# Performance work log

Measured on AMD Instinct MI355X. Metric: run time of the kernel, lower is better.

Reference implementation:

```python
import jax, jax.numpy as jnp
import numpy as np

B, C, L = 8, 64, 65536  # batch, channels, flattened H*W
GN_EPS = 1e-5


def setup_inputs() -> dict:
    key = jax.random.key(0)
    ks = jax.random.split(key, 8)
    return {
        "x": jax.random.normal(ks[0], (B, C, L), dtype=jnp.float32),
        "inj0": jax.random.normal(ks[1], (B, C, L), dtype=jnp.float32),
        "inj1": jax.random.normal(ks[2], (B, C, L), dtype=jnp.float32),
        "residual": jax.random.normal(ks[3], (B, C, L), dtype=jnp.float32),
        "gate_w": jax.random.normal(ks[4], (C, C), dtype=jnp.float32) * (1.0 / np.sqrt(C)),
        "gate_b": jax.random.normal(ks[5], (C,), dtype=jnp.float32) * 0.01,
        "fuse_w": jax.random.normal(ks[6], (C, C), dtype=jnp.float32) * (1.0 / np.sqrt(C)),
        "fuse_b": jax.random.normal(ks[7], (C,), dtype=jnp.float32) * 0.01,
        "gn_w": jnp.ones((C,), dtype=jnp.float32),
        "gn_b": jnp.zeros((C,), dtype=jnp.float32),
    }


def _conv1x1(w, b, t):
    # Conv1d with kernel_size=1: [O,C] x [B,C,L] -> [B,O,L]
    return jnp.einsum('oc,bcl->bol', w, t) + b[None, :, None]


def reference(x, inj0, inj1, residual, gate_w, gate_b, fuse_w, fuse_b, gn_w, gn_b):
    # per-injection gate + elementwise multiply, summed over injections
    acc = jnp.zeros_like(x)
    for inj in (inj0, inj1):  # fixed small list of injection features
        acc = acc + x * _conv1x1(gate_w, gate_b, inj + x)
    # fuse conv + residual + ReLU (dropout p=0 -> identity)
    out = jax.nn.relu(_conv1x1(fuse_w, fuse_b, acc) + residual)
    # GroupNorm(num_groups=1): normalize over (C, L) per sample, per-channel affine
    mean = jnp.mean(out, axis=(1, 2), keepdims=True)
    var = jnp.var(out, axis=(1, 2), keepdims=True)
    out = (out - mean) * jax.lax.rsqrt(var + GN_EPS)
    return out * gn_w[None, :, None] + gn_b[None, :, None]
```

## Files before the change

kernel.cpp:

```cpp
#include <hip/hip_runtime.h>
#include <stdint.h>

#define Bv 8
#define Cv 64
#define Lv 65536
#define TPB 512
#define COLS 256
#define BLKS_PER_B (Lv / COLS)
#define GRID1 (Bv * BLKS_PER_B)


typedef __attribute__((ext_vector_type(8))) short short8;
typedef __attribute__((ext_vector_type(4))) float f32x4;

#define SSTRIDE 260

__device__ __forceinline__ uint16_t f2bf(float f) {
    uint32_t u = __float_as_uint(f);
    uint32_t r = u + 0x7FFFu + ((u >> 16) & 1u);
    return (uint16_t)(r >> 16);
}
__device__ __forceinline__ uint32_t pack2bf(float lo, float hi) {
    return (uint32_t)f2bf(lo) | ((uint32_t)f2bf(hi) << 16);
}

__global__ void pass1(const float* __restrict__ x, const float* __restrict__ inj0,
                      const float* __restrict__ inj1, const float* __restrict__ resid,
                      const float* __restrict__ gate_w, const float* __restrict__ gate_b,
                      const float* __restrict__ fuse_w, const float* __restrict__ fuse_b,
                      float* __restrict__ out, float* __restrict__ partials)
{
    __shared__ uint32_t s_buf[32 * SSTRIDE];
    __shared__ uint32_t a_buf[16 * SSTRIDE];
    __shared__ uint32_t w_lds[2][64][36];
    __shared__ float cinit[2][64];
    __shared__ float wred[16];

    const int tid  = threadIdx.x;
    const int lane = tid & 63;
    const int w    = tid >> 6;
    const int g    = lane >> 4;
    const int ln   = lane & 15;

    const int b    = blockIdx.x >> 8;
    const int lb   = blockIdx.x & 255;
    const int col0 = lb * COLS;
    const int bCL  = b * (Cv * Lv);

    {
        const int mat = tid >> 8;
        const int m   = (tid >> 2) & 63;
        const int k0  = (tid & 3) << 4;
        const float* wsrc = mat ? fuse_w : gate_w;
        const float4* w4 = reinterpret_cast<const float4*>(wsrc + m * 64 + k0);
        uint32_t* dst = &w_lds[mat][m][k0 >> 1];
        #pragma unroll
        for (int q = 0; q < 4; ++q) {
            const float4 v = w4[q];
            dst[2 * q]     = pack2bf(v.x, v.y);
            dst[2 * q + 1] = pack2bf(v.z, v.w);
        }
        if (tid < 64) {
            cinit[0][tid] = 2.0f * gate_b[tid];
            cinit[1][tid] = fuse_b[tid];
        }
    }

    #pragma unroll
    for (int uu = 0; uu < 4; ++uu) {
        const int u  = tid + uu * TPB;
        const int kp = u >> 6;
        const int c  = (u & 63) << 2;
        const int rA = bCL + (2 * kp) * Lv + col0 + c;
        const int rB = rA + Lv;
        const float4 xA = *reinterpret_cast<const float4*>(x    + rA);
        const float4 aA = *reinterpret_cast<const float4*>(inj0 + rA);
        const float4 bA = *reinterpret_cast<const float4*>(inj1 + rA);
        const float4 xB = *reinterpret_cast<const float4*>(x    + rB);
        const float4 aB = *reinterpret_cast<const float4*>(inj0 + rB);
        const float4 bB = *reinterpret_cast<const float4*>(inj1 + rB);
        uint4 dw;
        dw.x = pack2bf(aA.x + bA.x + 2.0f * xA.x, aB.x + bB.x + 2.0f * xB.x);
        dw.y = pack2bf(aA.y + bA.y + 2.0f * xA.y, aB.y + bB.y + 2.0f * xB.y);
        dw.z = pack2bf(aA.z + bA.z + 2.0f * xA.z, aB.z + bB.z + 2.0f * xB.z);
        dw.w = pack2bf(aA.w + bA.w + 2.0f * xA.w, aB.w + bB.w + 2.0f * xB.w);
        *reinterpret_cast<uint4*>(&s_buf[kp * SSTRIDE + c]) = dw;
    }
    __syncthreads();

    f32x4 D2[4][2];
    #pragma unroll
    for (int oc = 0; oc < 4; ++oc) {
        const float4 cb = *reinterpret_cast<const float4*>(&cinit[1][16 * oc + 4 * g]);
        D2[oc][0][0] = cb.x; D2[oc][0][1] = cb.y;
        D2[oc][0][2] = cb.z; D2[oc][0][3] = cb.w;
        D2[oc][1] = D2[oc][0];
    }

    float lsum = 0.0f, lsq = 0.0f;

    #pragma unroll 1
    for (int ph = 0; ph < 2; ++ph) {
        f32x4 D1[2][2];
        #pragma unroll
        for (int o2 = 0; o2 < 2; ++o2) {
            const int oc = 2 * ph + o2;
            const float4 cb = *reinterpret_cast<const float4*>(&cinit[0][16 * oc + 4 * g]);
            D1[o2][0][0] = cb.x; D1[o2][0][1] = cb.y;
            D1[o2][0][2] = cb.z; D1[o2][0][3] = cb.w;
            D1[o2][1] = D1[o2][0];
        }
        #pragma unroll
        for (int nt = 0; nt < 2; ++nt) {
            const int n = ln + 16 * (2 * w + nt);
            uint4 B0, B1;
            B0.x = s_buf[(4 * g + 0) * SSTRIDE + n];
            B0.y = s_buf[(4 * g + 1) * SSTRIDE + n];
            B0.z = s_buf[(4 * g + 2) * SSTRIDE + n];
            B0.w = s_buf[(4 * g + 3) * SSTRIDE + n];
            B1.x = s_buf[(16 + 4 * g + 0) * SSTRIDE + n];
            B1.y = s_buf[(16 + 4 * g + 1) * SSTRIDE + n];
            B1.z = s_buf[(16 + 4 * g + 2) * SSTRIDE + n];
            B1.w = s_buf[(16 + 4 * g + 3) * SSTRIDE + n];
            #pragma unroll
            for (int o2 = 0; o2 < 2; ++o2) {
                const int m = ln + 16 * (2 * ph + o2);
                const uint4 A0 = *reinterpret_cast<const uint4*>(&w_lds[0][m][4 * g]);
                const uint4 A1 = *reinterpret_cast<const uint4*>(&w_lds[0][m][16 + 4 * g]);
                D1[o2][nt] = __builtin_amdgcn_mfma_f32_16x16x32_bf16(
                    __builtin_bit_cast(short8, A0), __builtin_bit_cast(short8, B0),
                    D1[o2][nt], 0, 0, 0);
                D1[o2][nt] = __builtin_amdgcn_mfma_f32_16x16x32_bf16(
                    __builtin_bit_cast(short8, A1), __builtin_bit_cast(short8, B1),
                    D1[o2][nt], 0, 0, 0);
            }
        }

        #pragma unroll
        for (int nt = 0; nt < 2; ++nt) {
            const int n  = ln + 16 * (2 * w + nt);
            const int cg = bCL + col0 + n;
            #pragma unroll
            for (int o2 = 0; o2 < 2; ++o2) {
                const int m0 = 16 * (2 * ph + o2) + 4 * g;
                float av[4];
                #pragma unroll
                for (int j = 0; j < 4; ++j)
                    av[j] = x[cg + (m0 + j) * Lv] * D1[o2][nt][j];
                const int kpA = 8 * o2 + 2 * g;
                a_buf[kpA * SSTRIDE + n]       = pack2bf(av[0], av[1]);
                a_buf[(kpA + 1) * SSTRIDE + n] = pack2bf(av[2], av[3]);
            }
        }
        __syncthreads();

        #pragma unroll
        for (int nt = 0; nt < 2; ++nt) {
            const int n = ln + 16 * (2 * w + nt);
            uint4 Bf;
            Bf.x = a_buf[(4 * g + 0) * SSTRIDE + n];
            Bf.y = a_buf[(4 * g + 1) * SSTRIDE + n];
            Bf.z = a_buf[(4 * g + 2) * SSTRIDE + n];
            Bf.w = a_buf[(4 * g + 3) * SSTRIDE + n];
            #pragma unroll
            for (int oc = 0; oc < 4; ++oc) {
                const int m = ln + 16 * oc;
                const uint4 A = *reinterpret_cast<const uint4*>(&w_lds[1][m][16 * ph + 4 * g]);
                D2[oc][nt] = __builtin_amdgcn_mfma_f32_16x16x32_bf16(
                    __builtin_bit_cast(short8, A), __builtin_bit_cast(short8, Bf),
                    D2[oc][nt], 0, 0, 0);
            }
        }
        __syncthreads();
    }

    {
        float* uf = reinterpret_cast<float*>(a_buf);
        const int rowin = tid >> 5;
        const int cl    = tid & 31;
        #pragma unroll
        for (int ck = 0; ck < 4; ++ck) {
            #pragma unroll
            for (int nt = 0; nt < 2; ++nt) {
                const int n = ln + 16 * (2 * w + nt);
                #pragma unroll
                for (int j = 0; j < 4; ++j)
                    uf[(4 * g + j) * SSTRIDE + n] = D2[ck][nt][j];
            }
            const int m   = 16 * ck + rowin;
            const int gbm = bCL + m * Lv + col0;
            const float4 ra = *reinterpret_cast<const float4*>(&resid[gbm + 4 * cl]);
            const float4 rb = *reinterpret_cast<const float4*>(&resid[gbm + 4 * cl + 128]);
            __syncthreads();
            float4 va = *reinterpret_cast<const float4*>(&uf[rowin * SSTRIDE + 4 * cl]);
            float4 vb = *reinterpret_cast<const float4*>(&uf[rowin * SSTRIDE + 4 * cl + 128]);
            va.x = fmaxf(va.x + ra.x, 0.0f); va.y = fmaxf(va.y + ra.y, 0.0f);
            va.z = fmaxf(va.z + ra.z, 0.0f); va.w = fmaxf(va.w + ra.w, 0.0f);
            vb.x = fmaxf(vb.x + rb.x, 0.0f); vb.y = fmaxf(vb.y + rb.y, 0.0f);
            vb.z = fmaxf(vb.z + rb.z, 0.0f); vb.w = fmaxf(vb.w + rb.w, 0.0f);
            *reinterpret_cast<float4*>(&out[gbm + 4 * cl])       = va;
            *reinterpret_cast<float4*>(&out[gbm + 4 * cl + 128]) = vb;
            lsum += (va.x + va.y) + (va.z + va.w) + (vb.x + vb.y) + (vb.z + vb.w);
            lsq = fmaf(va.x, va.x, lsq); lsq = fmaf(va.y, va.y, lsq);
            lsq = fmaf(va.z, va.z, lsq); lsq = fmaf(va.w, va.w, lsq);
            lsq = fmaf(vb.x, vb.x, lsq); lsq = fmaf(vb.y, vb.y, lsq);
            lsq = fmaf(vb.z, vb.z, lsq); lsq = fmaf(vb.w, vb.w, lsq);
            __syncthreads();
        }
    }

    #pragma unroll
    for (int st = 1; st < 64; st <<= 1) {
        lsum += __shfl_xor(lsum, st);
        lsq  += __shfl_xor(lsq,  st);
    }
    if (lane == 0) { wred[2 * w] = lsum; wred[2 * w + 1] = lsq; }
    __syncthreads();
    if (tid == 0) {
        float s = 0.0f, q = 0.0f;
        #pragma unroll
        for (int i = 0; i < 8; ++i) { s += wred[2 * i]; q += wred[2 * i + 1]; }
        partials[2 * blockIdx.x]     = s;
        partials[2 * blockIdx.x + 1] = q;
    }
}

__global__ __launch_bounds__(256)
void pass2(const float* __restrict__ partials, const float* __restrict__ gn_w,
           const float* __restrict__ gn_b, float* __restrict__ sb)
{
    __shared__ float r1[256], r2[256];
    __shared__ float mean_s, rs_s;
    const int b = blockIdx.x, tid = threadIdx.x;
    r1[tid] = partials[2 * (b * 256 + tid)];
    r2[tid] = partials[2 * (b * 256 + tid) + 1];
    __syncthreads();
    #pragma unroll
    for (int st = 128; st > 0; st >>= 1) {
        if (tid < st) { r1[tid] += r1[tid + st]; r2[tid] += r2[tid + st]; }
        __syncthreads();
    }
    if (tid == 0) {
        const float n = (float)Cv * (float)Lv;
        const float mean = r1[0] / n;
        const float var  = r2[0] / n - mean * mean;
        mean_s = mean;
        rs_s   = rsqrtf(var + 1e-5f);
    }
    __syncthreads();
    if (tid < Cv) {
        const float sc = gn_w[tid] * rs_s;
        sb[b * Cv + tid]           = sc;
        sb[Bv * Cv + b * Cv + tid] = fmaf(-mean_s, sc, gn_b[tid]);
    }
// ... 48 lines not shown
```

Measured before the change: 187.5 us.

## Process each block's columns in two halves to shrink LDS and registers

The 256-column tile per block is now processed as two sequential 128-column halves. Each wave owns one 16-column slice, and the separate a_buf is dropped by reusing s_buf for the intermediate product and the output staging. LDS use roughly halves and accumulator registers shrink, which should allow more resident blocks per CU to hide memory latency on this bandwidth-bound kernel. The cost is more barriers per block and less independent MFMA work per wave within each half.

```diff
diff --git a/kernel.cpp b/kernel.cpp
--- a/kernel.cpp
+++ b/kernel.cpp
@@ -5,6 +5,7 @@
 #define Cv 64
 #define Lv 65536
 #define TPB 512
+#define HALF 128
 #define COLS 256
 #define BLKS_PER_B (Lv / COLS)
 #define GRID1 (Bv * BLKS_PER_B)
@@ -13,7 +14,7 @@
 typedef __attribute__((ext_vector_type(8))) short short8;
 typedef __attribute__((ext_vector_type(4))) float f32x4;
 
-#define SSTRIDE 260
+#define SSTRIDE 132
 
 __device__ __forceinline__ uint16_t f2bf(float f) {
     uint32_t u = __float_as_uint(f);
@@ -31,7 +32,6 @@
                       float* __restrict__ out, float* __restrict__ partials)
 {
     __shared__ uint32_t s_buf[32 * SSTRIDE];
-    __shared__ uint32_t a_buf[16 * SSTRIDE];
     __shared__ uint32_t w_lds[2][64][36];
     __shared__ float cinit[2][64];
     __shared__ float wred[16];
@@ -41,10 +41,10 @@
     const int w    = tid >> 6;
     const int g    = lane >> 4;
     const int ln   = lane & 15;
+    const int n    = 16 * w + ln;
 
     const int b    = blockIdx.x >> 8;
     const int lb   = blockIdx.x & 255;
-    const int col0 = lb * COLS;
     const int bCL  = b * (Cv * Lv);
 
     {
@@ -66,53 +66,41 @@
         }
     }
 
-    #pragma unroll
-    for (int uu = 0; uu < 4; ++uu) {
-        const int u  = tid + uu * TPB;
-        const int kp = u >> 6;
-        const int c  = (u & 63) << 2;
-        const int rA = bCL + (2 * kp) * Lv + col0 + c;
-        const int rB = rA + Lv;
-        const float4 xA = *reinterpret_cast<const float4*>(x    + rA);
-        const float4 aA = *reinterpret_cast<const float4*>(inj0 + rA);
-        const float4 bA = *reinterpret_cast<const float4*>(inj1 + rA);
-        const float4 xB = *reinterpret_cast<const float4*>(x    + rB);
-        const float4 aB = *reinterpret_cast<const float4*>(inj0 + rB);
-        const float4 bB = *reinterpret_cast<const float4*>(inj1 + rB);
-        uint4 dw;
-        dw.x = pack2bf(aA.x + bA.x + 2.0f * xA.x, aB.x + bB.x + 2.0f * xB.x);
-        dw.y = pack2bf(aA.y + bA.y + 2.0f * xA.y, aB.y + bB.y + 2.0f * xB.y);
-        dw.z = pack2bf(aA.z + bA.z + 2.0f * xA.z, aB.z + bB.z + 2.0f * xB.z);
-        dw.w = pack2bf(aA.w + bA.w + 2.0f * xA.w, aB.w + bB.w + 2.0f * xB.w);
-        *reinterpret_cast<uint4*>(&s_buf[kp * SSTRIDE + c]) = dw;
-    }
-    __syncthreads();
-
-    f32x4 D2[4][2];
-    #pragma unroll
-    for (int oc = 0; oc < 4; ++oc) {
-        const float4 cb = *reinterpret_cast<const float4*>(&cinit[1][16 * oc + 4 * g]);
-        D2[oc][0][0] = cb.x; D2[oc][0][1] = cb.y;
-        D2[oc][0][2] = cb.z; D2[oc][0][3] = cb.w;
-        D2[oc][1] = D2[oc][0];
-    }
-
     float lsum = 0.0f, lsq = 0.0f;
 
     #pragma unroll 1
-    for (int ph = 0; ph < 2; ++ph) {
-        f32x4 D1[2][2];
-        #pragma unroll
-        for (int o2 = 0; o2 < 2; ++o2) {
-            const int oc = 2 * ph + o2;
+    for (int h = 0; h < 2; ++h) {
+        const int col0 = lb * COLS + h * HALF;
+
+        #pragma unroll
+        for (int uu = 0; uu < 2; ++uu) {
+            const int u  = tid + uu * TPB;
+            const int kp = u >> 5;
+            const int c  = (u & 31) << 2;
+            const int rA = bCL + (2 * kp) * Lv + col0 + c;
+            const int rB = rA + Lv;
+            const float4 xA = *reinterpret_cast<const float4*>(x    + rA);
+            const float4 aA = *reinterpret_cast<const float4*>(inj0 + rA);
+            const float4 bA = *reinterpret_cast<const float4*>(inj1 + rA);
+            const float4 xB = *reinterpret_cast<const float4*>(x    + rB);
+            const float4 aB = *reinterpret_cast<const float4*>(inj0 + rB);
+            const float4 bB = *reinterpret_cast<const float4*>(inj1 + rB);
+            uint4 dw;
+            dw.x = pack2bf(aA.x + bA.x + 2.0f * xA.x, aB.x + bB.x + 2.0f * xB.x);
+            dw.y = pack2bf(aA.y + bA.y + 2.0f * xA.y, aB.y + bB.y + 2.0f * xB.y);
+            dw.z = pack2bf(aA.z + bA.z + 2.0f * xA.z, aB.z + bB.z + 2.0f * xB.z);
+            dw.w = pack2bf(aA.w + bA.w + 2.0f * xA.w, aB.w + bB.w + 2.0f * xB.w);
+            *reinterpret_cast<uint4*>(&s_buf[kp * SSTRIDE + c]) = dw;
+        }
+        __syncthreads();
+
+        f32x4 D1[4];
+        #pragma unroll
+        for (int oc = 0; oc < 4; ++oc) {
             const float4 cb = *reinterpret_cast<const float4*>(&cinit[0][16 * oc + 4 * g]);
-            D1[o2][0][0] = cb.x; D1[o2][0][1] = cb.y;
-            D1[o2][0][2] = cb.z; D1[o2][0][3] = cb.w;
-            D1[o2][1] = D1[o2][0];
-        }
-        #pragma unroll
-        for (int nt = 0; nt < 2; ++nt) {
-            const int n = ln + 16 * (2 * w + nt);
+            D1[oc][0] = cb.x; D1[oc][1] = cb.y; D1[oc][2] = cb.z; D1[oc][3] = cb.w;
+        }
+        {
             uint4 B0, B1;
             B0.x = s_buf[(4 * g + 0) * SSTRIDE + n];
             B0.y = s_buf[(4 * g + 1) * SSTRIDE + n];
@@ -123,89 +111,99 @@
             B1.z = s_buf[(16 + 4 * g + 2) * SSTRIDE + n];
             B1.w = s_buf[(16 + 4 * g + 3) * SSTRIDE + n];
             #pragma unroll
-            for (int o2 = 0; o2 < 2; ++o2) {
-                const int m = ln + 16 * (2 * ph + o2);
+            for (int oc = 0; oc < 4; ++oc) {
+                const int m = ln + 16 * oc;
                 const uint4 A0 = *reinterpret_cast<const uint4*>(&w_lds[0][m][4 * g]);
                 const uint4 A1 = *reinterpret_cast<const uint4*>(&w_lds[0][m][16 + 4 * g]);
-                D1[o2][nt] = __builtin_amdgcn_mfma_f32_16x16x32_bf16(
+                D1[oc] = __builtin_amdgcn_mfma_f32_16x16x32_bf16(
                     __builtin_bit_cast(short8, A0), __builtin_bit_cast(short8, B0),
-                    D1[o2][nt], 0, 0, 0);
-                D1[o2][nt] = __builtin_amdgcn_mfma_f32_16x16x32_bf16(
+                    D1[oc], 0, 0, 0);
+                D1[oc] = __builtin_amdgcn_mfma_f32_16x16x32_bf16(
                     __builtin_bit_cast(short8, A1), __builtin_bit_cast(short8, B1),
-                    D1[o2][nt], 0, 0, 0);
+                    D1[oc], 0, 0, 0);
             }
         }
 
-        #pragma unroll
-        for (int nt = 0; nt < 2; ++nt) {
-            const int n  = ln + 16 * (2 * w + nt);
+        {
             const int cg = bCL + col0 + n;
             #pragma unroll
-            for (int o2 = 0; o2 < 2; ++o2) {
-                const int m0 = 16 * (2 * ph + o2) + 4 * g;
+            for (int oc = 0; oc < 4; ++oc) {
+                const int m0 = 16 * oc + 4 * g;
                 float av[4];
                 #pragma unroll
                 for (int j = 0; j < 4; ++j)
-                    av[j] = x[cg + (m0 + j) * Lv] * D1[o2][nt][j];
-                const int kpA = 8 * o2 + 2 * g;
-                a_buf[kpA * SSTRIDE + n]       = pack2bf(av[0], av[1]);
-                a_buf[(kpA + 1) * SSTRIDE + n] = pack2bf(av[2], av[3]);
+                    av[j] = x[cg + (m0 + j) * Lv] * D1[oc][j];
+                const int kp = 8 * oc + 2 * g;
+                s_buf[kp * SSTRIDE + n]       = pack2bf(av[0], av[1]);
+                s_buf[(kp + 1) * SSTRIDE + n] = pack2bf(av[2], av[3]);
             }
         }
         __syncthreads();
 
-        #pragma unroll
-        for (int nt = 0; nt < 2; ++nt) {
-            const int n = ln + 16 * (2 * w + nt);
-            uint4 Bf;
-            Bf.x = a_buf[(4 * g + 0) * SSTRIDE + n];
-            Bf.y = a_buf[(4 * g + 1) * SSTRIDE + n];
-            Bf.z = a_buf[(4 * g + 2) * SSTRIDE + n];
-            Bf.w = a_buf[(4 * g + 3) * SSTRIDE + n];
+        f32x4 D2[4];
+        #pragma unroll
+        for (int oc = 0; oc < 4; ++oc) {
+            const float4 cb = *reinterpret_cast<const float4*>(&cinit[1][16 * oc + 4 * g]);
+            D2[oc][0] = cb.x; D2[oc][1] = cb.y; D2[oc][2] = cb.z; D2[oc][3] = cb.w;
+        }
+        {
+            uint4 B0, B1;
+            B0.x = s_buf[(4 * g + 0) * SSTRIDE + n];
+            B0.y = s_buf[(4 * g + 1) * SSTRIDE + n];
+            B0.z = s_buf[(4 * g + 2) * SSTRIDE + n];
+            B0.w = s_buf[(4 * g + 3) * SSTRIDE + n];
+            B1.x = s_buf[(16 + 4 * g + 0) * SSTRIDE + n];
+            B1.y = s_buf[(16 + 4 * g + 1) * SSTRIDE + n];
+            B1.z = s_buf[(16 + 4 * g + 2) * SSTRIDE + n];
+            B1.w = s_buf[(16 + 4 * g + 3) * SSTRIDE + n];
             #pragma unroll
             for (int oc = 0; oc < 4; ++oc) {
                 const int m = ln + 16 * oc;
-                const uint4 A = *reinterpret_cast<const uint4*>(&w_lds[1][m][16 * ph + 4 * g]);
-                D2[oc][nt] = __builtin_amdgcn_mfma_f32_16x16x32_bf16(
-                    __builtin_bit_cast(short8, A), __builtin_bit_cast(short8, Bf),
-                    D2[oc][nt], 0, 0, 0);
+                const uint4 A0 = *reinterpret_cast<const uint4*>(&w_lds[1][m][4 * g]);
+                const uint4 A1 = *reinterpret_cast<const uint4*>(&w_lds[1][m][16 + 4 * g]);
+                D2[oc] = __builtin_amdgcn_mfma_f32_16x16x32_bf16(
+                    __builtin_bit_cast(short8, A0), __builtin_bit_cast(short8, B0),
+                    D2[oc], 0, 0, 0);
+                D2[oc] = __builtin_amdgcn_mfma_f32_16x16x32_bf16(
+                    __builtin_bit_cast(short8, A1), __builtin_bit_cast(short8, B1),
+                    D2[oc], 0, 0, 0);
             }
         }
         __syncthreads();
-    }
-
-    {
-        float* uf = reinterpret_cast<float*>(a_buf);
-        const int rowin = tid >> 5;
-        const int cl    = tid & 31;
-        #pragma unroll
-        for (int ck = 0; ck < 4; ++ck) {
-            #pragma unroll
-            for (int nt = 0; nt < 2; ++nt) {
-                const int n = ln + 16 * (2 * w + nt);
+
+        {
+            float* uf = reinterpret_cast<float*>(s_buf);
+            const int rowin = tid >> 4;
+            const int cl    = tid & 15;
+            #pragma unroll 1
+            for (int ck = 0; ck < 2; ++ck) {
                 #pragma unroll
-                for (int j = 0; j < 4; ++j)
-                    uf[(4 * g + j) * SSTRIDE + n] = D2[ck][nt][j];
+                for (int oc2 = 0; oc2 < 2; ++oc2) {
+                    const int oc = 2 * ck + oc2;
+                    #pragma unroll
+                    for (int j = 0; j < 4; ++j)
+                        uf[(16 * oc2 + 4 * g + j) * SSTRIDE + n] = D2[oc][j];
+                }
+                const int m   = 32 * ck + rowin;
+                const int gbm = bCL + m * Lv + col0;
+                const float4 ra = *reinterpret_cast<const float4*>(&resid[gbm + 4 * cl]);
+                const float4 rb = *reinterpret_cast<const float4*>(&resid[gbm + 4 * cl + 64]);
+                __syncthreads();
+                float4 va = *reinterpret_cast<const float4*>(&uf[rowin * SSTRIDE + 4 * cl]);
+                float4 vb = *reinterpret_cast<const float4*>(&uf[rowin * SSTRIDE + 4 * cl + 64]);
+                va.x = fmaxf(va.x + ra.x, 0.0f); va.y = fmaxf(va.y + ra.y, 0.0f);
+                va.z = fmaxf(va.z + ra.z, 0.0f); va.w = fmaxf(va.w + ra.w, 0.0f);
+                vb.x = fmaxf(vb.x + rb.x, 0.0f); vb.y = fmaxf(vb.y + rb.y, 0.0f);
+                vb.z = fmaxf(vb.z + rb.z, 0.0f); vb.w = fmaxf(vb.w + rb.w, 0.0f);
+                *reinterpret_cast<float4*>(&out[gbm + 4 * cl])      = va;
+                *reinterpret_cast<float4*>(&out[gbm + 4 * cl + 64]) = vb;
+                lsum += (va.x + va.y) + (va.z + va.w) + (vb.x + vb.y) + (vb.z + vb.w);
+                lsq = fmaf(va.x, va.x, lsq); lsq = fmaf(va.y, va.y, lsq);
+                lsq = fmaf(va.z, va.z, lsq); lsq = fmaf(va.w, va.w, lsq);
+                lsq = fmaf(vb.x, vb.x, lsq); lsq = fmaf(vb.y, vb.y, lsq);
+                lsq = fmaf(vb.z, vb.z, lsq); lsq = fmaf(vb.w, vb.w, lsq);
+                __syncthreads();
             }
-            const int m   = 16 * ck + rowin;
-            const int gbm = bCL + m * Lv + col0;
-            const float4 ra = *reinterpret_cast<const float4*>(&resid[gbm + 4 * cl]);
-            const float4 rb = *reinterpret_cast<const float4*>(&resid[gbm + 4 * cl + 128]);
-            __syncthreads();
-            float4 va = *reinterpret_cast<const float4*>(&uf[rowin * SSTRIDE + 4 * cl]);
-            float4 vb = *reinterpret_cast<const float4*>(&uf[rowin * SSTRIDE + 4 * cl + 128]);
-            va.x = fmaxf(va.x + ra.x, 0.0f); va.y = fmaxf(va.y + ra.y, 0.0f);
-            va.z = fmaxf(va.z + ra.z, 0.0f); va.w = fmaxf(va.w + ra.w, 0.0f);
-            vb.x = fmaxf(vb.x + rb.x, 0.0f); vb.y = fmaxf(vb.y + rb.y, 0.0f);
-            vb.z = fmaxf(vb.z + rb.z, 0.0f); vb.w = fmaxf(vb.w + rb.w, 0.0f);
-            *reinterpret_cast<float4*>(&out[gbm + 4 * cl])       = va;
-            *reinterpret_cast<float4*>(&out[gbm + 4 * cl + 128]) = vb;
-            lsum += (va.x + va.y) + (va.z + va.w) + (vb.x + vb.y) + (vb.z + vb.w);
-            lsq = fmaf(va.x, va.x, lsq); lsq = fmaf(va.y, va.y, lsq);
-            lsq = fmaf(va.z, va.z, lsq); lsq = fmaf(va.w, va.w, lsq);
-            lsq = fmaf(vb.x, vb.x, lsq); lsq = fmaf(vb.y, vb.y, lsq);
-            lsq = fmaf(vb.z, vb.z, lsq); lsq = fmaf(vb.w, vb.w, lsq);
-            __syncthreads();
         }
     }
 
```

Measured after the change: 191.4 us. 1.02x slower.

## Halve block size, process two column halves per block, load weights from global

Applied to the files above, without the earlier changes.

Cuts the block from 512 to 256 threads. Each block now handles its 256 columns in two 128-column halves, so the LDS tiles shrink to a 132-word stride. The bf16 weight tile in LDS is removed; each wave instead loads its MFMA A fragments directly from global gate_w/fuse_w (cached) and converts them to bf16 per phase. The goal is lower LDS use and higher occupancy, at the cost of repeated global weight loads and conversions and a serialized loop over the two halves.

```diff
diff --git a/kernel.cpp b/kernel.cpp
--- a/kernel.cpp
+++ b/kernel.cpp
@@ -4,7 +4,8 @@
 #define Bv 8
 #define Cv 64
 #define Lv 65536
-#define TPB 512
+#define TPB 256
+#define HALF 128
 #define COLS 256
 #define BLKS_PER_B (Lv / COLS)
 #define GRID1 (Bv * BLKS_PER_B)
@@ -13,7 +14,7 @@
 typedef __attribute__((ext_vector_type(8))) short short8;
 typedef __attribute__((ext_vector_type(4))) float f32x4;
 
-#define SSTRIDE 260
+#define SSTRIDE 132
 
 __device__ __forceinline__ uint16_t f2bf(float f) {
     uint32_t u = __float_as_uint(f);
@@ -22,6 +23,16 @@
 }
 __device__ __forceinline__ uint32_t pack2bf(float lo, float hi) {
     return (uint32_t)f2bf(lo) | ((uint32_t)f2bf(hi) << 16);
+}
+__device__ __forceinline__ uint4 load_wfrag(const float* wp) {
+    const float4 f0 = *reinterpret_cast<const float4*>(wp);
+    const float4 f1 = *reinterpret_cast<const float4*>(wp + 4);
+    uint4 r;
+    r.x = pack2bf(f0.x, f0.y);
+    r.y = pack2bf(f0.z, f0.w);
+    r.z = pack2bf(f1.x, f1.y);
+    r.w = pack2bf(f1.z, f1.w);
+    return r;
 }
 
 __global__ void pass1(const float* __restrict__ x, const float* __restrict__ inj0,
@@ -32,9 +43,8 @@
 {
     __shared__ uint32_t s_buf[32 * SSTRIDE];
     __shared__ uint32_t a_buf[16 * SSTRIDE];
-    __shared__ uint32_t w_lds[2][64][36];
     __shared__ float cinit[2][64];
-    __shared__ float wred[16];
+    __shared__ float wred[8];
 
     const int tid  = threadIdx.x;
     const int lane = tid & 63;
@@ -44,168 +54,169 @@
 
     const int b    = blockIdx.x >> 8;
     const int lb   = blockIdx.x & 255;
-    const int col0 = lb * COLS;
     const int bCL  = b * (Cv * Lv);
 
-    {
-        const int mat = tid >> 8;
-        const int m   = (tid >> 2) & 63;
-        const int k0  = (tid & 3) << 4;
-        const float* wsrc = mat ? fuse_w : gate_w;
-        const float4* w4 = reinterpret_cast<const float4*>(wsrc + m * 64 + k0);
-        uint32_t* dst = &w_lds[mat][m][k0 >> 1];
+    if (tid < 64) {
+        cinit[0][tid] = 2.0f * gate_b[tid];
+        cinit[1][tid] = fuse_b[tid];
+    }
+
+    float lsum = 0.0f, lsq = 0.0f;
+
+    #pragma unroll 1
+    for (int h = 0; h < 2; ++h) {
+        const int col0 = lb * COLS + h * HALF;
+
         #pragma unroll
-        for (int q = 0; q < 4; ++q) {
-            const float4 v = w4[q];
-            dst[2 * q]     = pack2bf(v.x, v.y);
-            dst[2 * q + 1] = pack2bf(v.z, v.w);
+        for (int uu = 0; uu < 4; ++uu) {
+            const int u  = tid + uu * TPB;
+            const int kp = u >> 5;
+            const int c  = (u & 31) << 2;
+            const int rA = bCL + (2 * kp) * Lv + col0 + c;
+            const int rB = rA + Lv;
+            const float4 xA = *reinterpret_cast<const float4*>(x    + rA);
+            const float4 aA = *reinterpret_cast<const float4*>(inj0 + rA);
+            const float4 bA = *reinterpret_cast<const float4*>(inj1 + rA);
+            const float4 xB = *reinterpret_cast<const float4*>(x    + rB);
+            const float4 aB = *reinterpret_cast<const float4*>(inj0 + rB);
+            const float4 bB = *reinterpret_cast<const float4*>(inj1 + rB);
+            uint4 dw;
+            dw.x = pack2bf(aA.x + bA.x + 2.0f * xA.x, aB.x + bB.x + 2.0f * xB.x);
+            dw.y = pack2bf(aA.y + bA.y + 2.0f * xA.y, aB.y + bB.y + 2.0f * xB.y);
+            dw.z = pack2bf(aA.z + bA.z + 2.0f * xA.z, aB.z + bB.z + 2.0f * xB.z);
+            dw.w = pack2bf(aA.w + bA.w + 2.0f * xA.w, aB.w + bB.w + 2.0f * xB.w);
+            *reinterpret_cast<uint4*>(&s_buf[kp * SSTRIDE + c]) = dw;
         }
-        if (tid < 64) {
-            cinit[0][tid] = 2.0f * gate_b[tid];
-            cinit[1][tid] = fuse_b[tid];
+        __syncthreads();
+
+        f32x4 D2[4][2];
+        #pragma unroll
+        for (int oc = 0; oc < 4; ++oc) {
+            const float4 cb = *reinterpret_cast<const float4*>(&cinit[1][16 * oc + 4 * g]);
+            D2[oc][0][0] = cb.x; D2[oc][0][1] = cb.y;
+            D2[oc][0][2] = cb.z; D2[oc][0][3] = cb.w;
+            D2[oc][1] = D2[oc][0];
         }
-    }
-
-    #pragma unroll
-    for (int uu = 0; uu < 4; ++uu) {
-        const int u  = tid + uu * TPB;
-        const int kp = u >> 6;
-        const int c  = (u & 63) << 2;
-        const int rA = bCL + (2 * kp) * Lv + col0 + c;
-        const int rB = rA + Lv;
-        const float4 xA = *reinterpret_cast<const float4*>(x    + rA);
-        const float4 aA = *reinterpret_cast<const float4*>(inj0 + rA);
-        const float4 bA = *reinterpret_cast<const float4*>(inj1 + rA);
-        const float4 xB = *reinterpret_cast<const float4*>(x    + rB);
-        const float4 aB = *reinterpret_cast<const float4*>(inj0 + rB);
-        const float4 bB = *reinterpret_cast<const float4*>(inj1 + rB);
-        uint4 dw;
-        dw.x = pack2bf(aA.x + bA.x + 2.0f * xA.x, aB.x + bB.x + 2.0f * xB.x);
-        dw.y = pack2bf(aA.y + bA.y + 2.0f * xA.y, aB.y + bB.y + 2.0f * xB.y);
-        dw.z = pack2bf(aA.z + bA.z + 2.0f * xA.z, aB.z + bB.z + 2.0f * xB.z);
-        dw.w = pack2bf(aA.w + bA.w + 2.0f * xA.w, aB.w + bB.w + 2.0f * xB.w);
-        *reinterpret_cast<uint4*>(&s_buf[kp * SSTRIDE + c]) = dw;
-    }
-    __syncthreads();
-
-    f32x4 D2[4][2];
-    #pragma unroll
-    for (int oc = 0; oc < 4; ++oc) {
-        const float4 cb = *reinterpret_cast<const float4*>(&cinit[1][16 * oc + 4 * g]);
-        D2[oc][0][0] = cb.x; D2[oc][0][1] = cb.y;
-        D2[oc][0][2] = cb.z; D2[oc][0][3] = cb.w;
-        D2[oc][1] = D2[oc][0];
-    }
-
-    float lsum = 0.0f, lsq = 0.0f;
-
-    #pragma unroll 1
-    for (int ph = 0; ph < 2; ++ph) {
-        f32x4 D1[2][2];
-        #pragma unroll
-        for (int o2 = 0; o2 < 2; ++o2) {
-            const int oc = 2 * ph + o2;
-            const float4 cb = *reinterpret_cast<const float4*>(&cinit[0][16 * oc + 4 * g]);
-            D1[o2][0][0] = cb.x; D1[o2][0][1] = cb.y;
-            D1[o2][0][2] = cb.z; D1[o2][0][3] = cb.w;
-            D1[o2][1] = D1[o2][0];
-        }
-        #pragma unroll
-        for (int nt = 0; nt < 2; ++nt) {
-            const int n = ln + 16 * (2 * w + nt);
-            uint4 B0, B1;
-            B0.x = s_buf[(4 * g + 0) * SSTRIDE + n];
-            B0.y = s_buf[(4 * g + 1) * SSTRIDE + n];
-            B0.z = s_buf[(4 * g + 2) * SSTRIDE + n];
-            B0.w = s_buf[(4 * g + 3) * SSTRIDE + n];
-            B1.x = s_buf[(16 + 4 * g + 0) * SSTRIDE + n];
-            B1.y = s_buf[(16 + 4 * g + 1) * SSTRIDE + n];
-            B1.z = s_buf[(16 + 4 * g + 2) * SSTRIDE + n];
-            B1.w = s_buf[(16 + 4 * g + 3) * SSTRIDE + n];
+
+        #pragma unroll 1
+        for (int ph = 0; ph < 2; ++ph) {
+            f32x4 D1[2][2];
             #pragma unroll
             for (int o2 = 0; o2 < 2; ++o2) {
-                const int m = ln + 16 * (2 * ph + o2);
-                const uint4 A0 = *reinterpret_cast<const uint4*>(&w_lds[0][m][4 * g]);
-                const uint4 A1 = *reinterpret_cast<const uint4*>(&w_lds[0][m][16 + 4 * g]);
-                D1[o2][nt] = __builtin_amdgcn_mfma_f32_16x16x32_bf16(
-                    __builtin_bit_cast(short8, A0), __builtin_bit_cast(short8, B0),
-                    D1[o2][nt], 0, 0, 0);
-                D1[o2][nt] = __builtin_amdgcn_mfma_f32_16x16x32_bf16(
-                    __builtin_bit_cast(short8, A1), __builtin_bit_cast(short8, B1),
-                    D1[o2][nt], 0, 0, 0);
-            }
-        }
-
-        #pragma unroll
-        for (int nt = 0; nt < 2; ++nt) {
-            const int n  = ln + 16 * (2 * w + nt);
-            const int cg = bCL + col0 + n;
-            #pragma unroll
-            for (int o2 = 0; o2 < 2; ++o2) {
-                const int m0 = 16 * (2 * ph + o2) + 4 * g;
-                float av[4];
-                #pragma unroll
-                for (int j = 0; j < 4; ++j)
-                    av[j] = x[cg + (m0 + j) * Lv] * D1[o2][nt][j];
-                const int kpA = 8 * o2 + 2 * g;
-                a_buf[kpA * SSTRIDE + n]       = pack2bf(av[0], av[1]);
-                a_buf[(kpA + 1) * SSTRIDE + n] = pack2bf(av[2], av[3]);
-            }
-        }
-        __syncthreads();
-
-        #pragma unroll
-        for (int nt = 0; nt < 2; ++nt) {
-            const int n = ln + 16 * (2 * w + nt);
-            uint4 Bf;
-            Bf.x = a_buf[(4 * g + 0) * SSTRIDE + n];
-            Bf.y = a_buf[(4 * g + 1) * SSTRIDE + n];
-            Bf.z = a_buf[(4 * g + 2) * SSTRIDE + n];
-            Bf.w = a_buf[(4 * g + 3) * SSTRIDE + n];
-            #pragma unroll
-            for (int oc = 0; oc < 4; ++oc) {
-                const int m = ln + 16 * oc;
-                const uint4 A = *reinterpret_cast<const uint4*>(&w_lds[1][m][16 * ph + 4 * g]);
-                D2[oc][nt] = __builtin_amdgcn_mfma_f32_16x16x32_bf16(
-                    __builtin_bit_cast(short8, A), __builtin_bit_cast(short8, Bf),
-                    D2[oc][nt], 0, 0, 0);
-            }
-        }
-        __syncthreads();
-    }
-
-    {
-        float* uf = reinterpret_cast<float*>(a_buf);
-        const int rowin = tid >> 5;
-        const int cl    = tid & 31;
-        #pragma unroll
-        for (int ck = 0; ck < 4; ++ck) {
+                const int oc = 2 * ph + o2;
+                const float4 cb = *reinterpret_cast<const float4*>(&cinit[0][16 * oc + 4 * g]);
+                D1[o2][0][0] = cb.x; D1[o2][0][1] = cb.y;
+                D1[o2][0][2] = cb.z; D1[o2][0][3] = cb.w;
+                D1[o2][1] = D1[o2][0];
+            }
+            {
+                uint4 A[2][2];
+                #pragma unroll
+                for (int o2 = 0; o2 < 2; ++o2) {
+                    const int m = ln + 16 * (2 * ph + o2);
+                    A[o2][0] = load_wfrag(gate_w + m * 64 + 8 * g);
+                    A[o2][1] = load_wfrag(gate_w + m * 64 + 32 + 8 * g);
+                }
+                #pragma unroll
+                for (int nt = 0; nt < 2; ++nt) {
+                    const int n = ln + 16 * (2 * w + nt);
+                    uint4 B0, B1;
+                    B0.x = s_buf[(4 * g + 0) * SSTRIDE + n];
+                    B0.y = s_buf[(4 * g + 1) * SSTRIDE + n];
+                    B0.z = s_buf[(4 * g + 2) * SSTRIDE + n];
+                    B0.w = s_buf[(4 * g + 3) * SSTRIDE + n];
+                    B1.x = s_buf[(16 + 4 * g + 0) * SSTRIDE + n];
+                    B1.y = s_buf[(16 + 4 * g + 1) * SSTRIDE + n];
+                    B1.z = s_buf[(16 + 4 * g + 2) * SSTRIDE + n];
+                    B1.w = s_buf[(16 + 4 * g + 3) * SSTRIDE + n];
+                    #pragma unroll
+                    for (int o2 = 0; o2 < 2; ++o2) {
+                        D1[o2][nt] = __builtin_amdgcn_mfma_f32_16x16x32_bf16(
+                            __builtin_bit_cast(short8, A[o2][0]),
+                            __builtin_bit_cast(short8, B0), D1[o2][nt], 0, 0, 0);
+                        D1[o2][nt] = __builtin_amdgcn_mfma_f32_16x16x32_bf16(
+                            __builtin_bit_cast(short8, A[o2][1]),
+                            __builtin_bit_cast(short8, B1), D1[o2][nt], 0, 0, 0);
+                    }
+                }
+            }
+
             #pragma unroll
             for (int nt = 0; nt < 2; ++nt) {
-                const int n = ln + 16 * (2 * w + nt);
-                #pragma unroll
-                for (int j = 0; j < 4; ++j)
-                    uf[(4 * g + j) * SSTRIDE + n] = D2[ck][nt][j];
-            }
-            const int m   = 16 * ck + rowin;
-            const int gbm = bCL + m * Lv + col0;
-            const float4 ra = *reinterpret_cast<const float4*>(&resid[gbm + 4 * cl]);
-            const float4 rb = *reinterpret_cast<const float4*>(&resid[gbm + 4 * cl + 128]);
+                const int n  = ln + 16 * (2 * w + nt);
+                const int cg = bCL + col0 + n;
+                #pragma unroll
+                for (int o2 = 0; o2 < 2; ++o2) {
+                    const int m0 = 16 * (2 * ph + o2) + 4 * g;
+                    float av[4];
+                    #pragma unroll
+                    for (int j = 0; j < 4; ++j)
+                        av[j] = x[cg + (m0 + j) * Lv] * D1[o2][nt][j];
+                    const int kpA = 8 * o2 + 2 * g;
+                    a_buf[kpA * SSTRIDE + n]       = pack2bf(av[0], av[1]);
+                    a_buf[(kpA + 1) * SSTRIDE + n] = pack2bf(av[2], av[3]);
+                }
+            }
             __syncthreads();
-            float4 va = *reinterpret_cast<const float4*>(&uf[rowin * SSTRIDE + 4 * cl]);
-            float4 vb = *reinterpret_cast<const float4*>(&uf[rowin * SSTRIDE + 4 * cl + 128]);
-            va.x = fmaxf(va.x + ra.x, 0.0f); va.y = fmaxf(va.y + ra.y, 0.0f);
-            va.z = fmaxf(va.z + ra.z, 0.0f); va.w = fmaxf(va.w + ra.w, 0.0f);
-            vb.x = fmaxf(vb.x + rb.x, 0.0f); vb.y = fmaxf(vb.y + rb.y, 0.0f);
-            vb.z = fmaxf(vb.z + rb.z, 0.0f); vb.w = fmaxf(vb.w + rb.w, 0.0f);
-            *reinterpret_cast<float4*>(&out[gbm + 4 * cl])       = va;
-            *reinterpret_cast<float4*>(&out[gbm + 4 * cl + 128]) = vb;
-            lsum += (va.x + va.y) + (va.z + va.w) + (vb.x + vb.y) + (vb.z + vb.w);
-            lsq = fmaf(va.x, va.x, lsq); lsq = fmaf(va.y, va.y, lsq);
-            lsq = fmaf(va.z, va.z, lsq); lsq = fmaf(va.w, va.w, lsq);
-            lsq = fmaf(vb.x, vb.x, lsq); lsq = fmaf(vb.y, vb.y, lsq);
-            lsq = fmaf(vb.z, vb.z, lsq); lsq = fmaf(vb.w, vb.w, lsq);
+
+            {
+                uint4 A2[4];
+                #pragma unroll
+                for (int oc = 0; oc < 4; ++oc) {
+                    const int m = ln + 16 * oc;
+                    A2[oc] = load_wfrag(fuse_w + m * 64 + 32 * ph + 8 * g);
+                }
+                #pragma unroll
+                for (int nt = 0; nt < 2; ++nt) {
+                    const int n = ln + 16 * (2 * w + nt);
+                    uint4 Bf;
+                    Bf.x = a_buf[(4 * g + 0) * SSTRIDE + n];
+                    Bf.y = a_buf[(4 * g + 1) * SSTRIDE + n];
+                    Bf.z = a_buf[(4 * g + 2) * SSTRIDE + n];
+                    Bf.w = a_buf[(4 * g + 3) * SSTRIDE + n];
+                    #pragma unroll
+                    for (int oc = 0; oc < 4; ++oc)
+                        D2[oc][nt] = __builtin_amdgcn_mfma_f32_16x16x32_bf16(
+                            __builtin_bit_cast(short8, A2[oc]),
+                            __builtin_bit_cast(short8, Bf), D2[oc][nt], 0, 0, 0);
+                }
+            }
             __syncthreads();
+        }
+
+        {
+            float* uf = reinterpret_cast<float*>(a_buf);
+            const int rowin = tid >> 4;
+            const int cl    = tid & 15;
+            #pragma unroll 1
+            for (int ck = 0; ck < 4; ++ck) {
+                #pragma unroll
+                for (int nt = 0; nt < 2; ++nt) {
+                    const int n = ln + 16 * (2 * w + nt);
+                    #pragma unroll
+                    for (int j = 0; j < 4; ++j)
+                        uf[(4 * g + j) * SSTRIDE + n] = D2[ck][nt][j];
+                }
+                const int m   = 16 * ck + rowin;
+                const int gbm = bCL + m * Lv + col0;
+                const float4 ra = *reinterpret_cast<const float4*>(&resid[gbm + 4 * cl]);
+                const float4 rb = *reinterpret_cast<const float4*>(&resid[gbm + 4 * cl + 64]);
+                __syncthreads();
+                float4 va = *reinterpret_cast<const float4*>(&uf[rowin * SSTRIDE + 4 * cl]);
+                float4 vb = *reinterpret_cast<const float4*>(&uf[rowin * SSTRIDE + 4 * cl + 64]);
+                va.x = fmaxf(va.x + ra.x, 0.0f); va.y = fmaxf(va.y + ra.y, 0.0f);
+                va.z = fmaxf(va.z + ra.z, 0.0f); va.w = fmaxf(va.w + ra.w, 0.0f);
+                vb.x = fmaxf(vb.x + rb.x, 0.0f); vb.y = fmaxf(vb.y + rb.y, 0.0f);
+                vb.z = fmaxf(vb.z + rb.z, 0.0f); vb.w = fmaxf(vb.w + rb.w, 0.0f);
+                *reinterpret_cast<float4*>(&out[gbm + 4 * cl])      = va;
+                *reinterpret_cast<float4*>(&out[gbm + 4 * cl + 64]) = vb;
+                lsum += (va.x + va.y) + (va.z + va.w) + (vb.x + vb.y) + (vb.z + vb.w);
+                lsq = fmaf(va.x, va.x, lsq); lsq = fmaf(va.y, va.y, lsq);
+                lsq = fmaf(va.z, va.z, lsq); lsq = fmaf(va.w, va.w, lsq);
+                lsq = fmaf(vb.x, vb.x, lsq); lsq = fmaf(vb.y, vb.y, lsq);
+                lsq = fmaf(vb.z, vb.z, lsq); lsq = fmaf(vb.w, vb.w, lsq);
+                __syncthreads();
+            }
         }
     }
 
@@ -219,7 +230,7 @@
     if (tid == 0) {
         float s = 0.0f, q = 0.0f;
         #pragma unroll
-        for (int i = 0; i < 8; ++i) { s += wred[2 * i]; q += wred[2 * i + 1]; }
+        for (int i = 0; i < 4; ++i) { s += wred[2 * i]; q += wred[2 * i + 1]; }
         partials[2 * blockIdx.x]     = s;
         partials[2 * blockIdx.x + 1] = q;
     }
```

Measured after the change: 212.9 us. +13.5%, slower.

## Give each wavefront private LDS slabs to drop block-wide barriers in fused conv

Applied to the files above, without the earlier changes.

Restructures pass1 so each of four wavefronts (256-thread blocks) owns a private 64-column slice, processed as two 32-column tiles with per-wave LDS slabs. This removes nearly all block-wide __syncthreads from the two-GEMM pipeline and the epilogue. It also caches x as bf16 in LDS instead of re-reading fp32 x from global memory for the gating multiply, and prefetches residual rows into registers ahead of the GEMMs. The cost is an extra rounding of x to bf16 in the gate product and fewer threads per block, which may reduce memory-level parallelism per block.

```diff
diff --git a/kernel.cpp b/kernel.cpp
--- a/kernel.cpp
+++ b/kernel.cpp
@@ -4,7 +4,8 @@
 #define Bv 8
 #define Cv 64
 #define Lv 65536
-#define TPB 512
+#define TPB 256
+#define WCOLS 32
 #define COLS 256
 #define BLKS_PER_B (Lv / COLS)
 #define GRID1 (Bv * BLKS_PER_B)
@@ -13,7 +14,7 @@
 typedef __attribute__((ext_vector_type(8))) short short8;
 typedef __attribute__((ext_vector_type(4))) float f32x4;
 
-#define SSTRIDE 260
+#define WS 36
 
 __device__ __forceinline__ uint16_t f2bf(float f) {
     uint32_t u = __float_as_uint(f);
@@ -23,6 +24,8 @@
 __device__ __forceinline__ uint32_t pack2bf(float lo, float hi) {
     return (uint32_t)f2bf(lo) | ((uint32_t)f2bf(hi) << 16);
 }
+__device__ __forceinline__ float bf_lo(uint32_t u) { return __uint_as_float(u << 16); }
+__device__ __forceinline__ float bf_hi(uint32_t u) { return __uint_as_float(u & 0xFFFF0000u); }
 
 __global__ void pass1(const float* __restrict__ x, const float* __restrict__ inj0,
                       const float* __restrict__ inj1, const float* __restrict__ resid,
@@ -30,11 +33,12 @@
                       const float* __restrict__ fuse_w, const float* __restrict__ fuse_b,
                       float* __restrict__ out, float* __restrict__ partials)
 {
-    __shared__ uint32_t s_buf[32 * SSTRIDE];
-    __shared__ uint32_t a_buf[16 * SSTRIDE];
-    __shared__ uint32_t w_lds[2][64][36];
+    __shared__ uint32_t w_lds[2][64][WS];
+    __shared__ uint32_t s_all[4][32 * WS];
+    __shared__ uint32_t x_all[4][32 * WS];
+    __shared__ uint32_t a_all[4][16 * WS];
     __shared__ float cinit[2][64];
-    __shared__ float wred[16];
+    __shared__ float wred[8];
 
     const int tid  = threadIdx.x;
     const int lane = tid & 63;
@@ -44,13 +48,18 @@
 
     const int b    = blockIdx.x >> 8;
     const int lb   = blockIdx.x & 255;
-    const int col0 = lb * COLS;
     const int bCL  = b * (Cv * Lv);
 
-    {
-        const int mat = tid >> 8;
-        const int m   = (tid >> 2) & 63;
-        const int k0  = (tid & 3) << 4;
+    uint32_t* s_slab = s_all[w];
+    uint32_t* x_slab = x_all[w];
+    uint32_t* a_slab = a_all[w];
+
+    #pragma unroll
+    for (int uu = 0; uu < 2; ++uu) {
+        const int unit = tid + uu * TPB;
+        const int mat  = unit >> 8;
+        const int m    = (unit >> 2) & 63;
+        const int k0   = (unit & 3) << 4;
         const float* wsrc = mat ? fuse_w : gate_w;
         const float4* w4 = reinterpret_cast<const float4*>(wsrc + m * 64 + k0);
         uint32_t* dst = &w_lds[mat][m][k0 >> 1];
@@ -60,152 +69,186 @@
             dst[2 * q]     = pack2bf(v.x, v.y);
             dst[2 * q + 1] = pack2bf(v.z, v.w);
         }
-        if (tid < 64) {
-            cinit[0][tid] = 2.0f * gate_b[tid];
-            cinit[1][tid] = fuse_b[tid];
-        }
-    }
-
-    #pragma unroll
-    for (int uu = 0; uu < 4; ++uu) {
-        const int u  = tid + uu * TPB;
-        const int kp = u >> 6;
-        const int c  = (u & 63) << 2;
-        const int rA = bCL + (2 * kp) * Lv + col0 + c;
-        const int rB = rA + Lv;
-        const float4 xA = *reinterpret_cast<const float4*>(x    + rA);
-        const float4 aA = *reinterpret_cast<const float4*>(inj0 + rA);
-        const float4 bA = *reinterpret_cast<const float4*>(inj1 + rA);
-        const float4 xB = *reinterpret_cast<const float4*>(x    + rB);
-        const float4 aB = *reinterpret_cast<const float4*>(inj0 + rB);
-        const float4 bB = *reinterpret_cast<const float4*>(inj1 + rB);
-        uint4 dw;
-        dw.x = pack2bf(aA.x + bA.x + 2.0f * xA.x, aB.x + bB.x + 2.0f * xB.x);
-        dw.y = pack2bf(aA.y + bA.y + 2.0f * xA.y, aB.y + bB.y + 2.0f * xB.y);
-        dw.z = pack2bf(aA.z + bA.z + 2.0f * xA.z, aB.z + bB.z + 2.0f * xB.z);
-        dw.w = pack2bf(aA.w + bA.w + 2.0f * xA.w, aB.w + bB.w + 2.0f * xB.w);
-        *reinterpret_cast<uint4*>(&s_buf[kp * SSTRIDE + c]) = dw;
+    }
+    if (tid < 64) {
+        cinit[0][tid] = 2.0f * gate_b[tid];
+        cinit[1][tid] = fuse_b[tid];
     }
     __syncthreads();
 
-    f32x4 D2[4][2];
-    #pragma unroll
-    for (int oc = 0; oc < 4; ++oc) {
-        const float4 cb = *reinterpret_cast<const float4*>(&cinit[1][16 * oc + 4 * g]);
-        D2[oc][0][0] = cb.x; D2[oc][0][1] = cb.y;
-        D2[oc][0][2] = cb.z; D2[oc][0][3] = cb.w;
-        D2[oc][1] = D2[oc][0];
-    }
-
     float lsum = 0.0f, lsq = 0.0f;
 
     #pragma unroll 1
-    for (int ph = 0; ph < 2; ++ph) {
-        f32x4 D1[2][2];
-        #pragma unroll
-        for (int o2 = 0; o2 < 2; ++o2) {
-            const int oc = 2 * ph + o2;
-            const float4 cb = *reinterpret_cast<const float4*>(&cinit[0][16 * oc + 4 * g]);
-            D1[o2][0][0] = cb.x; D1[o2][0][1] = cb.y;
-            D1[o2][0][2] = cb.z; D1[o2][0][3] = cb.w;
-            D1[o2][1] = D1[o2][0];
-        }
-        #pragma unroll
-        for (int nt = 0; nt < 2; ++nt) {
-            const int n = ln + 16 * (2 * w + nt);
-            uint4 B0, B1;
-            B0.x = s_buf[(4 * g + 0) * SSTRIDE + n];
-            B0.y = s_buf[(4 * g + 1) * SSTRIDE + n];
-            B0.z = s_buf[(4 * g + 2) * SSTRIDE + n];
-            B0.w = s_buf[(4 * g + 3) * SSTRIDE + n];
-            B1.x = s_buf[(16 + 4 * g + 0) * SSTRIDE + n];
-            B1.y = s_buf[(16 + 4 * g + 1) * SSTRIDE + n];
-            B1.z = s_buf[(16 + 4 * g + 2) * SSTRIDE + n];
-            B1.w = s_buf[(16 + 4 * g + 3) * SSTRIDE + n];
+    for (int t = 0; t < 2; ++t) {
+        const int col0w = lb * COLS + w * 64 + t * WCOLS;
+
+        #pragma unroll
+        for (int it = 0; it < 4; ++it) {
+            const int kp = 8 * it + (lane >> 3);
+            const int c  = (lane & 7) << 2;
+            const int rA = bCL + (2 * kp) * Lv + col0w + c;
+            const int rB = rA + Lv;
+            const float4 xA = *reinterpret_cast<const float4*>(x    + rA);
+            const float4 aA = *reinterpret_cast<const float4*>(inj0 + rA);
+            const float4 bA = *reinterpret_cast<const float4*>(inj1 + rA);
+            const float4 xB = *reinterpret_cast<const float4*>(x    + rB);
+            const float4 aB = *reinterpret_cast<const float4*>(inj0 + rB);
+            const float4 bB = *reinterpret_cast<const float4*>(inj1 + rB);
+            uint4 ds, dx;
+            ds.x = pack2bf(aA.x + bA.x + 2.0f * xA.x, aB.x + bB.x + 2.0f * xB.x);
+            ds.y = pack2bf(aA.y + bA.y + 2.0f * xA.y, aB.y + bB.y + 2.0f * xB.y);
+            ds.z = pack2bf(aA.z + bA.z + 2.0f * xA.z, aB.z + bB.z + 2.0f * xB.z);
+            ds.w = pack2bf(aA.w + bA.w + 2.0f * xA.w, aB.w + bB.w + 2.0f * xB.w);
+            *reinterpret_cast<uint4*>(&s_slab[kp * WS + c]) = ds;
+            dx.x = pack2bf(xA.x, xB.x);
+            dx.y = pack2bf(xA.y, xB.y);
+            dx.z = pack2bf(xA.z, xB.z);
+            dx.w = pack2bf(xA.w, xB.w);
+            *reinterpret_cast<uint4*>(&x_slab[kp * WS + c]) = dx;
+        }
+
+        float4 rp0[4];
+        #pragma unroll
+        for (int p = 0; p < 4; ++p) {
+            const int m = 8 * p + (lane >> 3);
+            rp0[p] = *reinterpret_cast<const float4*>(
+                &resid[bCL + m * Lv + col0w + ((lane & 7) << 2)]);
+        }
+
+        f32x4 D2[4][2];
+        #pragma unroll
+        for (int oc = 0; oc < 4; ++oc) {
+            const float4 cb = *reinterpret_cast<const float4*>(&cinit[1][16 * oc + 4 * g]);
+            D2[oc][0][0] = cb.x; D2[oc][0][1] = cb.y;
+            D2[oc][0][2] = cb.z; D2[oc][0][3] = cb.w;
+            D2[oc][1] = D2[oc][0];
+        }
+
+        #pragma unroll 1
+        for (int ph = 0; ph < 2; ++ph) {
+            f32x4 D1[2][2];
             #pragma unroll
             for (int o2 = 0; o2 < 2; ++o2) {
-                const int m = ln + 16 * (2 * ph + o2);
-                const uint4 A0 = *reinterpret_cast<const uint4*>(&w_lds[0][m][4 * g]);
-                const uint4 A1 = *reinterpret_cast<const uint4*>(&w_lds[0][m][16 + 4 * g]);
-                D1[o2][nt] = __builtin_amdgcn_mfma_f32_16x16x32_bf16(
-                    __builtin_bit_cast(short8, A0), __builtin_bit_cast(short8, B0),
-                    D1[o2][nt], 0, 0, 0);
-                D1[o2][nt] = __builtin_amdgcn_mfma_f32_16x16x32_bf16(
-                    __builtin_bit_cast(short8, A1), __builtin_bit_cast(short8, B1),
-                    D1[o2][nt], 0, 0, 0);
-            }
-        }
-
-        #pragma unroll
-        for (int nt = 0; nt < 2; ++nt) {
-            const int n  = ln + 16 * (2 * w + nt);
-            const int cg = bCL + col0 + n;
-            #pragma unroll
-            for (int o2 = 0; o2 < 2; ++o2) {
-                const int m0 = 16 * (2 * ph + o2) + 4 * g;
-                float av[4];
-                #pragma unroll
-                for (int j = 0; j < 4; ++j)
-                    av[j] = x[cg + (m0 + j) * Lv] * D1[o2][nt][j];
-                const int kpA = 8 * o2 + 2 * g;
-                a_buf[kpA * SSTRIDE + n]       = pack2bf(av[0], av[1]);
-                a_buf[(kpA + 1) * SSTRIDE + n] = pack2bf(av[2], av[3]);
-            }
-        }
-        __syncthreads();
-
-        #pragma unroll
-        for (int nt = 0; nt < 2; ++nt) {
-            const int n = ln + 16 * (2 * w + nt);
-            uint4 Bf;
-            Bf.x = a_buf[(4 * g + 0) * SSTRIDE + n];
-            Bf.y = a_buf[(4 * g + 1) * SSTRIDE + n];
-            Bf.z = a_buf[(4 * g + 2) * SSTRIDE + n];
-            Bf.w = a_buf[(4 * g + 3) * SSTRIDE + n];
-            #pragma unroll
-            for (int oc = 0; oc < 4; ++oc) {
-                const int m = ln + 16 * oc;
-                const uint4 A = *reinterpret_cast<const uint4*>(&w_lds[1][m][16 * ph + 4 * g]);
-                D2[oc][nt] = __builtin_amdgcn_mfma_f32_16x16x32_bf16(
-                    __builtin_bit_cast(short8, A), __builtin_bit_cast(short8, Bf),
-                    D2[oc][nt], 0, 0, 0);
-            }
-        }
-        __syncthreads();
-    }
-
-    {
-        float* uf = reinterpret_cast<float*>(a_buf);
-        const int rowin = tid >> 5;
-        const int cl    = tid & 31;
-        #pragma unroll
-        for (int ck = 0; ck < 4; ++ck) {
+                const int oc = 2 * ph + o2;
+                const float4 cb = *reinterpret_cast<const float4*>(&cinit[0][16 * oc + 4 * g]);
+                D1[o2][0][0] = cb.x; D1[o2][0][1] = cb.y;
+                D1[o2][0][2] = cb.z; D1[o2][0][3] = cb.w;
+                D1[o2][1] = D1[o2][0];
+            }
             #pragma unroll
             for (int nt = 0; nt < 2; ++nt) {
-                const int n = ln + 16 * (2 * w + nt);
-                #pragma unroll
-                for (int j = 0; j < 4; ++j)
-                    uf[(4 * g + j) * SSTRIDE + n] = D2[ck][nt][j];
-            }
-            const int m   = 16 * ck + rowin;
-            const int gbm = bCL + m * Lv + col0;
-            const float4 ra = *reinterpret_cast<const float4*>(&resid[gbm + 4 * cl]);
-            const float4 rb = *reinterpret_cast<const float4*>(&resid[gbm + 4 * cl + 128]);
-            __syncthreads();
-            float4 va = *reinterpret_cast<const float4*>(&uf[rowin * SSTRIDE + 4 * cl]);
-            float4 vb = *reinterpret_cast<const float4*>(&uf[rowin * SSTRIDE + 4 * cl + 128]);
-            va.x = fmaxf(va.x + ra.x, 0.0f); va.y = fmaxf(va.y + ra.y, 0.0f);
-            va.z = fmaxf(va.z + ra.z, 0.0f); va.w = fmaxf(va.w + ra.w, 0.0f);
-            vb.x = fmaxf(vb.x + rb.x, 0.0f); vb.y = fmaxf(vb.y + rb.y, 0.0f);
-            vb.z = fmaxf(vb.z + rb.z, 0.0f); vb.w = fmaxf(vb.w + rb.w, 0.0f);
-            *reinterpret_cast<float4*>(&out[gbm + 4 * cl])       = va;
-            *reinterpret_cast<float4*>(&out[gbm + 4 * cl + 128]) = vb;
-            lsum += (va.x + va.y) + (va.z + va.w) + (vb.x + vb.y) + (vb.z + vb.w);
-            lsq = fmaf(va.x, va.x, lsq); lsq = fmaf(va.y, va.y, lsq);
-            lsq = fmaf(va.z, va.z, lsq); lsq = fmaf(va.w, va.w, lsq);
-            lsq = fmaf(vb.x, vb.x, lsq); lsq = fmaf(vb.y, vb.y, lsq);
-            lsq = fmaf(vb.z, vb.z, lsq); lsq = fmaf(vb.w, vb.w, lsq);
-            __syncthreads();
+                const int n = ln + 16 * nt;
+                uint4 B0, B1;
+                B0.x = s_slab[(4 * g + 0) * WS + n];
+                B0.y = s_slab[(4 * g + 1) * WS + n];
+                B0.z = s_slab[(4 * g + 2) * WS + n];
+                B0.w = s_slab[(4 * g + 3) * WS + n];
+                B1.x = s_slab[(16 + 4 * g + 0) * WS + n];
+                B1.y = s_slab[(16 + 4 * g + 1) * WS + n];
+                B1.z = s_slab[(16 + 4 * g + 2) * WS + n];
+                B1.w = s_slab[(16 + 4 * g + 3) * WS + n];
+                #pragma unroll
+                for (int o2 = 0; o2 < 2; ++o2) {
+                    const int m = ln + 16 * (2 * ph + o2);
+                    const uint4 A0 = *reinterpret_cast<const uint4*>(&w_lds[0][m][4 * g]);
+                    const uint4 A1 = *reinterpret_cast<const uint4*>(&w_lds[0][m][16 + 4 * g]);
+                    D1[o2][nt] = __builtin_amdgcn_mfma_f32_16x16x32_bf16(
+                        __builtin_bit_cast(short8, A0), __builtin_bit_cast(short8, B0),
+                        D1[o2][nt], 0, 0, 0);
+                    D1[o2][nt] = __builtin_amdgcn_mfma_f32_16x16x32_bf16(
+                        __builtin_bit_cast(short8, A1), __builtin_bit_cast(short8, B1),
+                        D1[o2][nt], 0, 0, 0);
+                }
+            }
+
+            #pragma unroll
+            for (int nt = 0; nt < 2; ++nt) {
+                const int n = ln + 16 * nt;
+                #pragma unroll
+                for (int o2 = 0; o2 < 2; ++o2) {
+                    const int kpx = (16 * (2 * ph + o2) + 4 * g) >> 1;
+                    const uint32_t u0 = x_slab[kpx * WS + n];
+                    const uint32_t u1 = x_slab[(kpx + 1) * WS + n];
+                    float av[4];
+                    av[0] = bf_lo(u0) * D1[o2][nt][0];
+                    av[1] = bf_hi(u0) * D1[o2][nt][1];
+                    av[2] = bf_lo(u1) * D1[o2][nt][2];
+                    av[3] = bf_hi(u1) * D1[o2][nt][3];
+                    const int kpA = 8 * o2 + 2 * g;
+                    a_slab[kpA * WS + n]       = pack2bf(av[0], av[1]);
+                    a_slab[(kpA + 1) * WS + n] = pack2bf(av[2], av[3]);
+                }
+            }
+
+            #pragma unroll
+            for (int nt = 0; nt < 2; ++nt) {
+                const int n = ln + 16 * nt;
+                uint4 Bf;
+                Bf.x = a_slab[(4 * g + 0) * WS + n];
+                Bf.y = a_slab[(4 * g + 1) * WS + n];
+                Bf.z = a_slab[(4 * g + 2) * WS + n];
+                Bf.w = a_slab[(4 * g + 3) * WS + n];
+                #pragma unroll
+                for (int oc = 0; oc < 4; ++oc) {
+                    const int m = ln + 16 * oc;
+                    const uint4 A2 = *reinterpret_cast<const uint4*>(
+                        &w_lds[1][m][16 * ph + 4 * g]);
+                    D2[oc][nt] = __builtin_amdgcn_mfma_f32_16x16x32_bf16(
+                        __builtin_bit_cast(short8, A2), __builtin_bit_cast(short8, Bf),
+                        D2[oc][nt], 0, 0, 0);
+                }
+            }
+        }
+
+        {
+            float* uf = reinterpret_cast<float*>(s_slab);
+            const int rr = lane >> 3;
+            const int c4 = (lane & 7) << 2;
+            #pragma unroll 1
+            for (int ck = 0; ck < 2; ++ck) {
+                float4 rp1[4];
+                if (ck == 0) {
+                    #pragma unroll
+                    for (int p = 0; p < 4; ++p) {
+                        const int m = 32 + 8 * p + rr;
+                        rp1[p] = *reinterpret_cast<const float4*>(
+                            &resid[bCL + m * Lv + col0w + c4]);
+                    }
+                }
+                #pragma unroll
+                for (int o2 = 0; o2 < 2; ++o2) {
+                    const int oc = 2 * ck + o2;
+                    #pragma unroll
+                    for (int nt = 0; nt < 2; ++nt) {
+                        const int n = ln + 16 * nt;
+                        #pragma unroll
+                        for (int j = 0; j < 4; ++j)
+                            uf[(16 * o2 + 4 * g + j) * WS + n] = D2[oc][nt][j];
+                    }
+                }
+                #pragma unroll
+                for (int p = 0; p < 4; ++p) {
+                    const int r   = 8 * p + rr;
+                    const int m   = 32 * ck + r;
+                    const int gbm = bCL + m * Lv + col0w + c4;
+                    float4 v = *reinterpret_cast<const float4*>(&uf[r * WS + c4]);
+                    const float4 rv = rp0[p];
+                    v.x = fmaxf(v.x + rv.x, 0.0f);
+                    v.y = fmaxf(v.y + rv.y, 0.0f);
+                    v.z = fmaxf(v.z + rv.z, 0.0f);
+                    v.w = fmaxf(v.w + rv.w, 0.0f);
+                    *reinterpret_cast<float4*>(&out[gbm]) = v;
+                    lsum += (v.x + v.y) + (v.z + v.w);
+                    lsq = fmaf(v.x, v.x, lsq);
+                    lsq = fmaf(v.y, v.y, lsq);
+                    lsq = fmaf(v.z, v.z, lsq);
+                    lsq = fmaf(v.w, v.w, lsq);
+                }
+                if (ck == 0) {
+                    #pragma unroll
+                    for (int p = 0; p < 4; ++p) rp0[p] = rp1[p];
+                }
+            }
         }
     }
 
@@ -219,7 +262,7 @@
     if (tid == 0) {
         float s = 0.0f, q = 0.0f;
         #pragma unroll
-        for (int i = 0; i < 8; ++i) { s += wred[2 * i]; q += wred[2 * i + 1]; }
+        for (int i = 0; i < 4; ++i) { s += wred[2 * i]; q += wred[2 * i + 1]; }
         partials[2 * blockIdx.x]     = s;
         partials[2 * blockIdx.x + 1] = q;
     }
```

Measured after the change: 240.0 us. 1.28x slower.
